# Kernel optimization log

Hardware: AMD Instinct MI355X
Metric: run time of the kernel (lower is better)

## Reference

```python
import jax, jax.numpy as jnp
import numpy as np

N = 8192   # nodes in each graph (N1 must equal N2: V is built from x1)
D = 512    # output_dim


def setup_inputs() -> dict:
    key = jax.random.key(0)
    k1, k2, kq, kk, kv = jax.random.split(key, 5)
    std = 1.0 / np.sqrt(D)
    return {
        "x1": jax.random.normal(k1, (N, D), dtype=jnp.float32),
        "x2": jax.random.normal(k2, (N, D), dtype=jnp.float32),
        "q": jax.random.uniform(kq, (D, D), dtype=jnp.float32, minval=-std, maxval=std),
        "k": jax.random.uniform(kk, (D, D), dtype=jnp.float32, minval=-std, maxval=std),
        "v": jax.random.uniform(kv, (D, D), dtype=jnp.float32, minval=-std, maxval=std),
    }


def reference(x1, x2, q, k, v):
    Q = x1 @ q                       # [N, D]
    V = x1 @ v                       # [N, D]  (note: V from x1, as in the original)
    K = x2 @ k                       # [N, D]
    e = jax.nn.leaky_relu(Q @ K.T, negative_slope=0.01)  # [N, N]
    attention = jax.nn.softmax(e, axis=-1)
    return attention @ V             # [N, D]
```

## Files before the change

kernel.cpp:

```cpp
#include <hip/hip_runtime.h>
#include <hip/hip_bf16.h>

typedef unsigned short u16;
typedef unsigned int u32;
typedef float floatx4 __attribute__((ext_vector_type(4)));
typedef _Float16 f16x8 __attribute__((ext_vector_type(8)));

#define NN 8192
#define DD 512
#define NPARTS 4
#define JCHUNK 2048
#define RB_PER_PART 64

__device__ __forceinline__ u16 f2h(float f) {
    _Float16 h = (_Float16)f;
    return __builtin_bit_cast(u16, h);
}
__device__ __forceinline__ float h2f(u16 u) {
    _Float16 h = __builtin_bit_cast(_Float16, u);
    return (float)h;
}

__device__ __forceinline__ void async16(const u16* g, u16* l) {
    __builtin_amdgcn_global_load_lds(
        (const __attribute__((address_space(1))) u32*)g,
        (__attribute__((address_space(3))) u32*)l, 16, 0, 0);
}

__global__ __launch_bounds__(256)
void prep_kernel(const float* __restrict__ x1, const float* __restrict__ x2,
                 const float* __restrict__ qw, const float* __restrict__ kw,
                 const float* __restrict__ vw,
                 u16* __restrict__ x1h, u16* __restrict__ x2h,
                 u16* __restrict__ qT, u16* __restrict__ kT,
                 u16* __restrict__ vT, int* __restrict__ cnt)
{
    const int t = blockIdx.x * 256 + threadIdx.x;
    const int stride = gridDim.x * 256;
    if (t < NPARTS) cnt[t] = 0;

    const int NQ = NN * DD / 4;
    for (int i = t; i < NQ; i += stride) {
        float4 f = ((const float4*)x1)[i];
        ushort4 h;
        h.x = f2h(f.x); h.y = f2h(f.y); h.z = f2h(f.z); h.w = f2h(f.w);
        ((ushort4*)x1h)[i] = h;
        f = ((const float4*)x2)[i];
        h.x = f2h(f.x); h.y = f2h(f.y); h.z = f2h(f.z); h.w = f2h(f.w);
        ((ushort4*)x2h)[i] = h;
    }
    const int NW = DD * DD;
    for (int i = t; i < NW; i += stride) {
        const int k = i >> 9, n = i & 511;
        qT[n * DD + k] = f2h(qw[i]);
        kT[n * DD + k] = f2h(kw[i]);
        vT[n * DD + k] = f2h(vw[i]);
    }
}

__global__ __launch_bounds__(256, 2)
void proj_kernel(const u16* __restrict__ x1h, const u16* __restrict__ x2h,
                 const u16* __restrict__ qT, const u16* __restrict__ kT,
                 const u16* __restrict__ vT,
                 u16* __restrict__ Qf, u16* __restrict__ Kf, u16* __restrict__ VT)
{
    const int which = blockIdx.z;
    const u16* A = (which == 1) ? x2h : x1h;
    const u16* W = (which == 0) ? qT : (which == 1 ? kT : vT);

    __shared__ u16 Ab[2][128 * 64];
    __shared__ u16 Wb[2][128 * 64];

    const int tid  = threadIdx.x;
    const int lane = tid & 63;
    const int wave = tid >> 6;
    const int l15  = lane & 15;
    const int quad = lane >> 4;
    const int wm   = (wave & 1) * 64;
    const int wn   = (wave >> 1) * 64;
    const int m0   = blockIdx.x * 128;
    const int n0   = blockIdx.y * 128;

    const int vrs = lane >> 3;
    const int vch = (lane & 7) ^ vrs;
    int sOff[4];
    for (int i = 0; i < 4; i++) {
        const int c = wave * 4 + i;
        sOff[i] = (c * 8 + vrs) * DD + vch * 8;
    }

    auto stage = [&](int buf, int k0) {
        const u16* a = A + (size_t)m0 * DD + k0;
        const u16* w = W + (size_t)n0 * DD + k0;
        u16* da = &Ab[buf][wave * 2048];
        u16* dw = &Wb[buf][wave * 2048];
        async16(a + sOff[0], da);
        async16(a + sOff[1], da + 512);
        async16(a + sOff[2], da + 1024);
        async16(a + sOff[3], da + 1536);
        async16(w + sOff[0], dw);
        async16(w + sOff[1], dw + 512);
        async16(w + sOff[2], dw + 1024);
        async16(w + sOff[3], dw + 1536);
        __builtin_amdgcn_sched_barrier(0);
    };

    floatx4 acc[4][4] = {};

    stage(0, 0);
    asm volatile("s_waitcnt vmcnt(0)" ::: "memory");
    __syncthreads();

    for (int t = 0; t < 8; t++) {
        if (t < 7) stage((t & 1) ^ 1, (t + 1) * 64);
        const int buf = t & 1;
        __builtin_amdgcn_s_setprio(1);
        for (int ks = 0; ks < 2; ks++) {
            f16x8 af[4], bf[4];
            for (int mi = 0; mi < 4; mi++) {
                const int row = wm + mi * 16 + l15;
                const int ch  = (ks * 4 + quad) ^ (l15 & 7);
                af[mi] = *(const f16x8*)&Ab[buf][row * 64 + ch * 8];
            }
            for (int ni = 0; ni < 4; ni++) {
                const int row = wn + ni * 16 + l15;
                const int ch  = (ks * 4 + quad) ^ (l15 & 7);
                bf[ni] = *(const f16x8*)&Wb[buf][row * 64 + ch * 8];
            }
            for (int mi = 0; mi < 4; mi++)
                for (int ni = 0; ni < 4; ni++)
                    acc[mi][ni] = __builtin_amdgcn_mfma_f32_16x16x32_f16(
                        af[mi], bf[ni], acc[mi][ni], 0, 0, 0);
        }
        __builtin_amdgcn_s_setprio(0);
        asm volatile("s_waitcnt vmcnt(0)" ::: "memory");
        __syncthreads();
    }

    for (int mi = 0; mi < 4; mi++)
        for (int ni = 0; ni < 4; ni++)
            for (int r = 0; r < 4; r++) {
                const int row = m0 + wm + mi * 16 + quad * 4 + r;
                const int col = n0 + wn + ni * 16 + l15;
                const u16 hv = f2h(acc[mi][ni][r]);
                if (which == 0)      Qf[(size_t)row * DD + col] = hv;
                else if (which == 1) Kf[(size_t)row * DD + col] = hv;
                else                 VT[(size_t)col * NN + row] = hv;
            }
}

__global__ __launch_bounds__(512, 2)
void attn_kernel(const u16* __restrict__ Qf, const u16* __restrict__ Kf,
                 const u16* __restrict__ VT,
                 u16* __restrict__ Opart, float* __restrict__ Mp,
                 float* __restrict__ Lp, int* __restrict__ cnt)
{
    const int tid  = threadIdx.x;
    const int lane = tid & 63;
    const int wave = tid >> 6;
    const int w3   = wave & 3;
    const int wsel = wave >> 2;
    const int l15  = lane & 15;
    const int quad = lane >> 4;

    __shared__ u16 KV[6][8192];
    __shared__ u16 Ps[8][16 * 68];
    __shared__ int sPart, sRb;

    if (tid == 0) {
        u32 xcd;
        asm volatile("s_getreg_b32 %0, hwreg(HW_REG_XCC_ID)" : "=s"(xcd));
        xcd &= 3;
        int part = -1, rb = 0;
        for (int t = 0; t < 4; t++) {
            const int p = (xcd + t) & 3;
            const int idx = atomicAdd(&cnt[p], 1);
            if (idx < RB_PER_PART) { part = p; rb = idx; break; }
        }
        sPart = part; sRb = rb;
    }
    __syncthreads();
    const int part = sPart;
    const int rb   = sRb;
    if (part < 0) return;

    const int q0 = rb * 128 + wave * 16;

    f16x8 qf[16];
    for (int kk = 0; kk < 16; kk++)
        qf[kk] = *(const f16x8*)&Qf[(size_t)(q0 + l15) * DD + kk * 32 + quad * 8];

    floatx4 o[32] = {};
    float m_run[4], l_run[4];
    for (int r = 0; r < 4; r++) { m_run[r] = -1e30f; l_run[r] = 0.f; }

    const int j_begin = part * JCHUNK;
    const int j_end   = j_begin + JCHUNK;

    const int krow4  = lane >> 4;
    const int kpos16 = lane & 15;
    const int vrs    = lane >> 3;
    const int vch    = (lane & 7) ^ vrs;

    int kOff[4], vOff[4];
    for (int i = 0; i < 4; i++) {
        const int c    = w3 * 4 + i;
        const int krow = c * 4 + krow4;
        kOff[i] = krow * DD + (kpos16 ^ (krow & 7)) * 8;
        vOff[i] = (c * 8 + vrs) * NN + vch * 8;
    }

    auto stageK = [&](int dq, int j0, int slot) {
        const u16* b = Kf + (size_t)j0 * DD + dq * 128;
        u16* d = &KV[slot][w3 * 2048];
        async16(b + kOff[0], d);
        async16(b + kOff[1], d + 512);
        async16(b + kOff[2], d + 1024);
        async16(b + kOff[3], d + 1536);
        __builtin_amdgcn_sched_barrier(0);
    };
    auto stageV = [&](int dq, int j0, int slot) {
        const u16* b = VT + (size_t)dq * 128 * NN + j0;
        u16* d = &KV[slot][w3 * 2048];
        async16(b + vOff[0], d);
        async16(b + vOff[1], d + 512);
        async16(b + vOff[2], d + 1024);
        async16(b + vOff[3], d + 1536);
        __builtin_amdgcn_sched_barrier(0);
    };

    auto qkQ = [&](int rg, int dq, floatx4* s) {
        __builtin_amdgcn_s_setprio(1);
        for (int k8 = 0; k8 < 4; k8++)
            for (int nt = 0; nt < 4; nt++) {
                const int row = nt * 16 + l15;
                const int ch  = (k8 * 4 + quad) ^ (l15 & 7);
                f16x8 b = *(const f16x8*)&KV[rg][row * 128 + ch * 8];
                s[nt] = __builtin_amdgcn_mfma_f32_16x16x32_f16(qf[dq * 4 + k8], b, s[nt], 0, 0, 0);
            }
        __builtin_amdgcn_s_setprio(0);
    };
    auto pvQ = [&](int rg, int dq) {
        f16x8 pf0 = *(const f16x8*)&Ps[wave][l15 * 68 + quad * 8];
        f16x8 pf1 = *(const f16x8*)&Ps[wave][l15 * 68 + 32 + quad * 8];
        __builtin_amdgcn_s_setprio(1);
        for (int t = 0; t < 8; t++) {
            const int row = t * 16 + l15;
            const int c0  = quad ^ (l15 & 7);
            const int c1  = (4 + quad) ^ (l15 & 7);
            f16x8 b0 = *(const f16x8*)&KV[rg][row * 64 + c0 * 8];
            f16x8 b1 = *(const f16x8*)&KV[rg][row * 64 + c1 * 8];
            o[dq * 8 + t] = __builtin_amdgcn_mfma_f32_16x16x32_f16(pf0, b0, o[dq * 8 + t], 0, 0, 0);
            o[dq * 8 + t] = __builtin_amdgcn_mfma_f32_16x16x32_f16(pf1, b1, o[dq * 8 + t], 0, 0, 0);
        }
        __builtin_amdgcn_s_setprio(0);
    };

    auto pbar = [&]() {
        asm volatile("s_waitcnt vmcnt(4)" ::: "memory");
        asm volatile("s_barrier" ::: "memory");
    };
    auto wrap6 = [](int x) { return x >= 6 ? x - 6 : x; };

    if (wsel == 0) stageK(0, j_begin, 0); else stageK(1, j_begin, 1);
    if (wsel == 0) stageK(2, j_begin, 2); else stageK(3, j_begin, 3);
    asm volatile("s_waitcnt vmcnt(0)" ::: "memory");
    asm volatile("s_barrier" ::: "memory");

    int sc = 4;

    for (int j0 = j_begin; j0 < j_end; j0 += 64) {
        const int jn = (j0 + 64 < j_end) ? j0 + 64 : j_begin;
        floatx4 s[4] = {};
        int sA, sB, cA, cB;

        sA = sc; sB = sc + 1; cA = wrap6(sc + 2); cB = cA + 1; sc = cA;
        if (wsel == 0) stageV(0, j0, sA); else stageV(1, j0, sB);
        qkQ(cA, 0, s);
        qkQ(cB, 1, s);
        pbar();

        sA = sc; sB = sc + 1; cA = wrap6(sc + 2); cB = cA + 1; sc = cA;
        if (wsel == 0) stageV(2, j0, sA); else stageV(3, j0, sB);
        qkQ(cA, 2, s);
        qkQ(cB, 3, s);

        for (int nt = 0; nt < 4; nt++)
            for (int r = 0; r < 4; r++) {
                float x = s[nt][r];
                s[nt][r] = x >= 0.f ? x : 0.01f * x;
            }
        float mt[4];
        for (int r = 0; r < 4; r++)
            mt[r] = fmaxf(fmaxf(s[0][r], s[1][r]), fmaxf(s[2][r], s[3][r]));
        for (int off = 1; off < 16; off <<= 1)
            for (int r = 0; r < 4; r++)
                mt[r] = fmaxf(mt[r], __shfl_xor(mt[r], off));

        float alpha[4];
        for (int r = 0; r < 4; r++) {
            const float mnew = fmaxf(m_run[r], mt[r]);
            alpha[r] = __expf(m_run[r] - mnew);
            m_run[r] = mnew;
        }
        float ls[4] = {0.f, 0.f, 0.f, 0.f};
        u16 pv[4][4];
        for (int nt = 0; nt < 4; nt++)
            for (int r = 0; r < 4; r++) {
                const float p = __expf(s[nt][r] - m_run[r]);
                ls[r] += p;
                pv[nt][r] = f2h(p);
            }
        for (int off = 1; off < 16; off <<= 1)
            for (int r = 0; r < 4; r++)
                ls[r] += __shfl_xor(ls[r], off);
        for (int r = 0; r < 4; r++)
            l_run[r] = l_run[r] * alpha[r] + ls[r];
        const bool need = (alpha[0] != 1.f) | (alpha[1] != 1.f) |
                          (alpha[2] != 1.f) | (alpha[3] != 1.f);
        if (__any(need))
            for (int i = 0; i < 32; i++)
                for (int r = 0; r < 4; r++)
                    o[i][r] *= alpha[r];

        for (int nt = 0; nt < 4; nt++)
            for (int r = 0; r < 4; r++)
                Ps[wave][(quad * 4 + r) * 68 + nt * 16 + l15] = pv[nt][r];
        asm volatile("s_waitcnt lgkmcnt(0)" ::: "memory");

        pbar();

        sA = sc; sB = sc + 1; cA = wrap6(sc + 2); cB = cA + 1; sc = cA;
        if (wsel == 0) stageK(0, jn, sA); else stageK(1, jn, sB);
        pvQ(cA, 0);
        pvQ(cB, 1);
        pbar();

        sA = sc; sB = sc + 1; cA = wrap6(sc + 2); cB = cA + 1; sc = cA;
        if (wsel == 0) stageK(2, jn, sA); else stageK(3, jn, sB);
        pvQ(cA, 2);
        pvQ(cB, 3);
        pbar();
    }

    asm volatile("s_waitcnt vmcnt(0)" ::: "memory");

    for (int i = 0; i < 32; i++)
        for (int r = 0; r < 4; r++) {
            const int row = q0 + quad * 4 + r;
            const int col = i * 16 + l15;
            Opart[((size_t)part * NN + row) * DD + col] = f2h(o[i][r]);
        }
    if (l15 == 0)
        for (int r = 0; r < 4; r++) {
            const int row = q0 + quad * 4 + r;
            Mp[part * NN + row] = m_run[r];
            Lp[part * NN + row] = l_run[r];
        }
}

__global__ __launch_bounds__(256)
void combine_kernel(const u16* __restrict__ Opart, const float* __restrict__ Mp,
                    const float* __restrict__ Lp, float* __restrict__ out)
{
    const int t   = blockIdx.x * 256 + threadIdx.x;
    const int row = t >> 6;
    const int c0  = (t & 63) * 8;

    float m[NPARTS], l[NPARTS];
    float M = -1e30f;
    for (int p = 0; p < NPARTS; p++) {
        m[p] = Mp[p * NN + row];
        l[p] = Lp[p * NN + row];
        M = fmaxf(M, m[p]);
    }
    float w[NPARTS], L = 0.f;
    for (int p = 0; p < NPARTS; p++) { w[p] = __expf(m[p] - M); L += w[p] * l[p]; }
    const float inv = 1.f / L;

    float acc[8] = {};
    for (int p = 0; p < NPARTS; p++) {
        f16x8 v = *(const f16x8*)&Opart[((size_t)p * NN + row) * DD + c0];
        for (int j = 0; j < 8; j++)
            acc[j] += w[p] * (float)v[j];
    }
    float4 o0, o1;
    o0.x = acc[0] * inv; o0.y = acc[1] * inv; o0.z = acc[2] * inv; o0.w = acc[3] * inv;
    o1.x = acc[4] * inv; o1.y = acc[5] * inv; o1.z = acc[6] * inv; o1.w = acc[7] * inv;
    *(float4*)&out[(size_t)row * DD + c0]     = o0;
    *(float4*)&out[(size_t)row * DD + c0 + 4] = o1;
}

extern "C" void kernel_launch(void* const* d_in, const int* in_sizes, int n_in,
                              void* d_out, int out_size, void* d_ws, size_t ws_size,
                              hipStream_t stream)
{
    const float* x1 = (const float*)d_in[0];
    const float* x2 = (const float*)d_in[1];
    const float* qw = (const float*)d_in[2];
    const float* kw = (const float*)d_in[3];
    const float* vw = (const float*)d_in[4];
    float* out = (float*)d_out;

    u16* Qf = (u16*)d_ws;
    u16* Kf = Qf + (size_t)NN * DD;
    u16* VT = Kf + (size_t)NN * DD;
    u16* Opart = VT + (size_t)NN * DD;
    float* Mp = (float*)(Opart + (size_t)NPARTS * NN * DD);
    float* Lp = Mp + NPARTS * NN;
    int* cnt = (int*)(Lp + NPARTS * NN);
    u16* x1h = (u16*)(cnt + 8);
    u16* x2h = x1h + (size_t)NN * DD;
    u16* qT  = x2h + (size_t)NN * DD;
    u16* kT  = qT + DD * DD;
    u16* vT  = kT + DD * DD;

    prep_kernel<<<1024, 256, 0, stream>>>(x1, x2, qw, kw, vw,
                                          x1h, x2h, qT, kT, vT, cnt);
    proj_kernel<<<dim3(64, 4, 3), 256, 0, stream>>>(x1h, x2h, qT, kT, vT,
                                                    Qf, Kf, VT);
    attn_kernel<<<dim3(RB_PER_PART * NPARTS), 512, 0, stream>>>(Qf, Kf, VT, Opart, Mp, Lp, cnt);
    combine_kernel<<<(NN * 64) / 256, 256, 0, stream>>>(Opart, Mp, Lp, out);
}
```

Baseline: 364.6 us.

## Repartition PV matmul so each wave owns a D-column slice across all rows

The P·V stage is reorganised so each wave computes a 64-column slice of the output for all 128 query rows. Previously each wave computed its own 16 rows across all 512 columns. V fragments are loaded from LDS once per wave and reused across the 8 row tiles, while P tiles from every wave are read from shared memory. Per-row softmax rescale factors are passed through a new LDS array and applied per tile, and the rotating 6-slot K/V ring becomes fixed slots in an 8-slot buffer with adjusted waitcnt barriers. This aims to cut redundant LDS reads of V, but it adds more LDS usage, drops the skip-if-alpha-is-1 shortcut, and may reduce load/compute overlap.

```diff
diff --git a/kernel.cpp b/kernel.cpp
--- a/kernel.cpp
+++ b/kernel.cpp
@@ -163,8 +163,9 @@
     const int l15  = lane & 15;
     const int quad = lane >> 4;
 
-    __shared__ u16 KV[6][8192];
+    __shared__ u16 KV[8][8192];
     __shared__ u16 Ps[8][16 * 68];
+    __shared__ float Als[128];
     __shared__ int sPart, sRb;
 
     if (tid == 0) {
@@ -240,66 +241,82 @@
             }
         __builtin_amdgcn_s_setprio(0);
     };
-    auto pvQ = [&](int rg, int dq) {
-        f16x8 pf0 = *(const f16x8*)&Ps[wave][l15 * 68 + quad * 8];
-        f16x8 pf1 = *(const f16x8*)&Ps[wave][l15 * 68 + 32 + quad * 8];
+
+    auto pvHalf = [&](int mb) {
+        const int rV    = 4 + (wave >> 1);
+        const int dbase = (wave & 1) * 64;
+        f16x8 bf0[4], bf1[4];
+        #pragma unroll
+        for (int nt = 0; nt < 4; nt++) {
+            const int dl = dbase + nt * 16 + l15;
+            const int c0 = quad ^ (l15 & 7);
+            const int c1 = (4 + quad) ^ (l15 & 7);
+            bf0[nt] = *(const f16x8*)&KV[rV][dl * 64 + c0 * 8];
+            bf1[nt] = *(const f16x8*)&KV[rV][dl * 64 + c1 * 8];
+        }
         __builtin_amdgcn_s_setprio(1);
-        for (int t = 0; t < 8; t++) {
-            const int row = t * 16 + l15;
-            const int c0  = quad ^ (l15 & 7);
-            const int c1  = (4 + quad) ^ (l15 & 7);
-            f16x8 b0 = *(const f16x8*)&KV[rg][row * 64 + c0 * 8];
-            f16x8 b1 = *(const f16x8*)&KV[rg][row * 64 + c1 * 8];
-            o[dq * 8 + t] = __builtin_amdgcn_mfma_f32_16x16x32_f16(pf0, b0, o[dq * 8 + t], 0, 0, 0);
-            o[dq * 8 + t] = __builtin_amdgcn_mfma_f32_16x16x32_f16(pf1, b1, o[dq * 8 + t], 0, 0, 0);
+        #pragma unroll
+        for (int m4 = 0; m4 < 4; m4++) {
+            const int mt = mb + m4;
+            f16x8 a0 = *(const f16x8*)&Ps[mt][l15 * 68 + quad * 8];
+            f16x8 a1 = *(const f16x8*)&Ps[mt][l15 * 68 + 32 + quad * 8];
+            float alr[4];
+            #pragma unroll
+            for (int r = 0; r < 4; r++)
+                alr[r] = Als[mt * 16 + quad * 4 + r];
+            #pragma unroll
+            for (int nt = 0; nt < 4; nt++) {
+                #pragma unroll
+                for (int r = 0; r < 4; r++)
+                    o[mt * 4 + nt][r] *= alr[r];
+                o[mt * 4 + nt] = __builtin_amdgcn_mfma_f32_16x16x32_f16(
+                    a0, bf0[nt], o[mt * 4 + nt], 0, 0, 0);
+                o[mt * 4 + nt] = __builtin_amdgcn_mfma_f32_16x16x32_f16(
+                    a1, bf1[nt], o[mt * 4 + nt], 0, 0, 0);
+            }
         }
         __builtin_amdgcn_s_setprio(0);
     };
 
-    auto pbar = [&]() {
-        asm volatile("s_waitcnt vmcnt(4)" ::: "memory");
-        asm volatile("s_barrier" ::: "memory");
-    };
-    auto wrap6 = [](int x) { return x >= 6 ? x - 6 : x; };
-
-    if (wsel == 0) stageK(0, j_begin, 0); else stageK(1, j_begin, 1);
-    if (wsel == 0) stageK(2, j_begin, 2); else stageK(3, j_begin, 3);
-    asm volatile("s_waitcnt vmcnt(0)" ::: "memory");
-    asm volatile("s_barrier" ::: "memory");
-
-    int sc = 4;
+    auto bar8 = [&]() { asm volatile("s_waitcnt vmcnt(8)" ::: "memory");
+                        asm volatile("s_barrier" ::: "memory"); };
+    auto bar4 = [&]() { asm volatile("s_waitcnt vmcnt(4)" ::: "memory");
+                        asm volatile("s_barrier" ::: "memory"); };
+    auto bar0 = [&]() { asm volatile("s_waitcnt vmcnt(0)" ::: "memory");
+                        asm volatile("s_barrier" ::: "memory"); };
+
+    if (wsel == 0) { stageK(0, j_begin, 0); stageK(2, j_begin, 2); }
+    else           { stageK(1, j_begin, 1); stageK(3, j_begin, 3); }
+    bar0();
 
     for (int j0 = j_begin; j0 < j_end; j0 += 64) {
         const int jn = (j0 + 64 < j_end) ? j0 + 64 : j_begin;
         floatx4 s[4] = {};
-        int sA, sB, cA, cB;
-
-        sA = sc; sB = sc + 1; cA = wrap6(sc + 2); cB = cA + 1; sc = cA;
-        if (wsel == 0) stageV(0, j0, sA); else stageV(1, j0, sB);
-        qkQ(cA, 0, s);
-        qkQ(cB, 1, s);
-        pbar();
-
-        sA = sc; sB = sc + 1; cA = wrap6(sc + 2); cB = cA + 1; sc = cA;
-        if (wsel == 0) stageV(2, j0, sA); else stageV(3, j0, sB);
-        qkQ(cA, 2, s);
-        qkQ(cB, 3, s);
+
+        if (wsel == 0) { stageV(0, j0, 4); stageV(1, j0, 5); }
+        else           { stageV(2, j0, 6); stageV(3, j0, 7); }
+        qkQ(0, 0, s);
+        qkQ(1, 1, s);
+        bar8();
+
+        qkQ(2, 2, s);
+        qkQ(3, 3, s);
 
         for (int nt = 0; nt < 4; nt++)
             for (int r = 0; r < 4; r++) {
                 float x = s[nt][r];
                 s[nt][r] = x >= 0.f ? x : 0.01f * x;
             }
-        float mt[4];
+        float mt4[4];
         for (int r = 0; r < 4; r++)
-            mt[r] = fmaxf(fmaxf(s[0][r], s[1][r]), fmaxf(s[2][r], s[3][r]));
+            mt4[r] = fmaxf(fmaxf(s[0][r], s[1][r]), fmaxf(s[2][r], s[3][r]));
         for (int off = 1; off < 16; off <<= 1)
             for (int r = 0; r < 4; r++)
-                mt[r] = fmaxf(mt[r], __shfl_xor(mt[r], off));
+                mt4[r] = fmaxf(mt4[r], __shfl_xor(mt4[r], off));
 
         float alpha[4];
         for (int r = 0; r < 4; r++) {
-            const float mnew = fmaxf(m_run[r], mt[r]);
+            const float mnew = fmaxf(m_run[r], mt4[r]);
             alpha[r] = __expf(m_run[r] - mnew);
             m_run[r] = mnew;
         }
@@ -316,41 +333,35 @@
                 ls[r] += __shfl_xor(ls[r], off);
         for (int r = 0; r < 4; r++)
             l_run[r] = l_run[r] * alpha[r] + ls[r];
-        const bool need = (alpha[0] != 1.f) | (alpha[1] != 1.f) |
-                          (alpha[2] != 1.f) | (alpha[3] != 1.f);
-        if (__any(need))
-            for (int i = 0; i < 32; i++)
-                for (int r = 0; r < 4; r++)
-                    o[i][r] *= alpha[r];
+
+        if (l15 == 0)
+            for (int r = 0; r < 4; r++)
+                Als[wave * 16 + quad * 4 + r] = alpha[r];
 
         for (int nt = 0; nt < 4; nt++)
             for (int r = 0; r < 4; r++)
                 Ps[wave][(quad * 4 + r) * 68 + nt * 16 + l15] = pv[nt][r];
         asm volatile("s_waitcnt lgkmcnt(0)" ::: "memory");
-
-        pbar();
-
-        sA = sc; sB = sc + 1; cA = wrap6(sc + 2); cB = cA + 1; sc = cA;
-        if (wsel == 0) stageK(0, jn, sA); else stageK(1, jn, sB);
-        pvQ(cA, 0);
-        pvQ(cB, 1);
-        pbar();
-
-        sA = sc; sB = sc + 1; cA = wrap6(sc + 2); cB = cA + 1; sc = cA;
-        if (wsel == 0) stageK(2, jn, sA); else stageK(3, jn, sB);
-        pvQ(cA, 2);
-        pvQ(cB, 3);
-        pbar();
+        bar0();
+
+        if (wsel == 0) stageK(0, jn, 0); else stageK(1, jn, 1);
+        pvHalf(0);
+        bar4();
+
+        if (wsel == 0) stageK(2, jn, 2); else stageK(3, jn, 3);
+        pvHalf(4);
+        bar4();
     }
 
     asm volatile("s_waitcnt vmcnt(0)" ::: "memory");
 
-    for (int i = 0; i < 32; i++)
-        for (int r = 0; r < 4; r++) {
-            const int row = q0 + quad * 4 + r;
-            const int col = i * 16 + l15;
-            Opart[((size_t)part * NN + row) * DD + col] = f2h(o[i][r]);
-        }
+    for (int mt = 0; mt < 8; mt++)
+        for (int nt = 0; nt < 4; nt++)
+            for (int r = 0; r < 4; r++) {
+                const int row = rb * 128 + mt * 16 + quad * 4 + r;
+                const int col = wave * 64 + nt * 16 + l15;
+                Opart[((size_t)part * NN + row) * DD + col] = f2h(o[mt * 4 + nt][r]);
+            }
     if (l15 == 0)
         for (int r = 0; r < 4; r++) {
             const int row = q0 + quad * 4 + r;
```

After: 441.0 us. +21.0%, slower.
